# Kernel tuning notes

Measured on AMD Instinct MI355X. Metric: run time of the kernel, lower is better.

Reference implementation:

```python
import jax, jax.numpy as jnp
import numpy as np

NEG_SLOPE = 0.01  # torch F.leaky_relu default


def _gat_stack(x, W, a1w, a1b, a2w, a2b):
    """One GAT stack over all heads.
    x: (B, N, F_in); W: (H, F_in, d); a1w/a2w: (H, d); a1b/a2b: (H,)
    returns (B, N, H*d) -- heads concatenated in order along last dim.
    """
    # 1x1 conv1d (no bias) == per-node linear projection
    fts = jnp.einsum('bnf,hfd->hbnd', x, W)                      # (H,B,N,d)
    f1 = jnp.einsum('hbnd,hd->hbn', fts, a1w) + a1b[:, None, None]
    f2 = jnp.einsum('hbnd,hd->hbn', fts, a2w) + a2b[:, None, None]
    # logits[h,b,i,j] = f1[h,b,i] + f2[h,b,j]  (f_1.permute + f_2 broadcast)
    logits = f1[:, :, :, None] + f2[:, :, None, :]               # (H,B,N,N)
    coefs = jax.nn.softmax(jax.nn.leaky_relu(logits, NEG_SLOPE), axis=-1)
    vals = jnp.einsum('hbnm,hbmd->hbnd', coefs, fts)             # bmm aggregation
    ret = jax.nn.elu(vals + fts)                                 # residual-within-head + ELU activation
    B, N = x.shape[0], x.shape[1]
    return jnp.transpose(ret, (1, 2, 0, 3)).reshape(B, N, -1)    # cat(heads, dim=-1)


def setup_inputs() -> dict:
    key = jax.random.key(0)
    ks = jax.random.split(key, 7)
    B, N, F_in, H, d = 32, 512, 128, 8, 64
    hidden = H * d  # 512
    s = 0.05
    return {
        'x':   jax.random.normal(ks[0], (B, N, F_in), jnp.float32),
        'W0':  jax.random.normal(ks[1], (H, F_in, d), jnp.float32) * s,
        'W1':  jax.random.normal(ks[2], (H, hidden, d), jnp.float32) * s,
        'a1w': jax.random.normal(ks[3], (2, H, d), jnp.float32) * s,
        'a1b': jax.random.normal(ks[4], (2, H), jnp.float32) * s,
        'a2w': jax.random.normal(ks[5], (2, H, d), jnp.float32) * s,
        'a2b': jax.random.normal(ks[6], (2, H), jnp.float32) * s,
    }


def reference(x, W0, W1, a1w, a1b, a2w, a2b):
    # stack 0: input dim = num_random_sample
    h = _gat_stack(x, W0, a1w[0], a1b[0], a2w[0], a2b[0])
    # stack 1: input dim = hidden_dim
    out = _gat_stack(h, W1, a1w[1], a1b[1], a2w[1], a2b[1])
    return out
```

## Files before the change

### kernel.cpp

```cpp
#include <hip/hip_runtime.h>
#include <hip/hip_bf16.h>
#include <stdint.h>

typedef __attribute__((ext_vector_type(8))) short short8;
typedef __attribute__((ext_vector_type(4))) float f32x4;

#define L2E 1.44269504f
#define FN  131072

__device__ __forceinline__ short f2bf(float f) {
    unsigned u = __builtin_bit_cast(unsigned, f);
    return (short)((u + 0x8000u) >> 16);
}
__device__ __forceinline__ float bf2f(short s) {
    unsigned u = ((unsigned)(unsigned short)s) << 16;
    return __builtin_bit_cast(float, u);
}

__device__ __forceinline__ void gld16(void* l, const void* g) {
    __builtin_amdgcn_global_load_lds(
        (const __attribute__((address_space(1))) unsigned*)g,
        (__attribute__((address_space(3))) unsigned*)l, 16, 0, 0);
}

__global__ void wtrans_kernel(const float* __restrict__ W0, const float* __restrict__ W1,
                              short* __restrict__ BT0, short* __restrict__ BT1) {
    int idx = blockIdx.x * 256 + threadIdx.x;
    if (idx < 8 * 128 * 64) {
        int h = idx >> 13;
        int k = (idx >> 6) & 127;
        int dd = idx & 63;
        BT0[(h * 64 + dd) * 128 + k] = f2bf(W0[idx]);
    } else {
        int j = idx - 8 * 128 * 64;
        int h = j >> 15;
        int k = (j >> 6) & 511;
        int dd = j & 63;
        BT1[(h * 64 + dd) * 512 + k] = f2bf(W1[j]);
    }
}

template <typename AT>
__global__ __launch_bounds__(256, 2)
void gemm_kernel(const AT* __restrict__ A, const short* __restrict__ BT,
                 short* __restrict__ fts, int K,
                 const float* __restrict__ a1w, const float* __restrict__ a1b,
                 const float* __restrict__ a2w, const float* __restrict__ a2b,
                 float* __restrict__ fbuf) {
    __shared__ __align__(16) short As[128 * 64];
    __shared__ __align__(16) short Bs[128 * 64];

    const int tid  = threadIdx.x;
    const int lane = tid & 63;
    const int w    = tid >> 6;
    const int wr   = w >> 1, wc = w & 1;
    const int quad = lane >> 4, l15 = lane & 15;
    const int m0   = blockIdx.y * 128;
    const int n0   = blockIdx.x * 128;

    const int rl   = lane >> 3;
    const int cpos = lane & 7;
    const int kcl  = cpos ^ rl;

    f32x4 acc[4][4];
    for (int i = 0; i < 4; ++i)
        for (int j = 0; j < 4; ++j) { f32x4 z = {0.f, 0.f, 0.f, 0.f}; acc[i][j] = z; }

    const int nkb = K >> 6;
    for (int kb = 0; kb < nkb; ++kb) {
        __syncthreads();
        if constexpr (sizeof(AT) == 4) {
            for (int i = 0; i < 8; ++i) {
                int id  = tid + i * 256;
                int row = id >> 4, q = id & 15;
                int c = q >> 1, half = q & 1;
                float4 v = *(const float4*)((const float*)A + (size_t)(m0 + row) * K + kb * 64 + q * 4);
                ushort4 p;
                p.x = (unsigned short)f2bf(v.x);
                p.y = (unsigned short)f2bf(v.y);
                p.z = (unsigned short)f2bf(v.z);
                p.w = (unsigned short)f2bf(v.w);
                int swz = c ^ (row & 7);
                *(ushort4*)(As + row * 64 + swz * 8 + half * 4) = p;
            }
        } else {
            for (int i = 0; i < 4; ++i) {
                int rowb = w * 32 + i * 8;
                gld16(As + rowb * 64,
                      (const short*)A + (size_t)(m0 + rowb + rl) * K + kb * 64 + kcl * 8);
            }
        }
        for (int i = 0; i < 4; ++i) {
            int rowb = w * 32 + i * 8;
            gld16(Bs + rowb * 64,
                  BT + (size_t)(n0 + rowb + rl) * K + kb * 64 + kcl * 8);
        }
        __syncthreads();
        short8 af[2][4], bf[2][4];
        for (int ks = 0; ks < 2; ++ks) {
            for (int mf = 0; mf < 4; ++mf) {
                int row = wr * 64 + mf * 16 + l15;
                af[ks][mf] = *(const short8*)(As + row * 64 + (((ks * 4 + quad) ^ (row & 7)) << 3));
            }
            for (int nf = 0; nf < 4; ++nf) {
                int row = wc * 64 + nf * 16 + l15;
                bf[ks][nf] = *(const short8*)(Bs + row * 64 + (((ks * 4 + quad) ^ (row & 7)) << 3));
            }
        }
        for (int ks = 0; ks < 2; ++ks)
            for (int mf = 0; mf < 4; ++mf)
                for (int nf = 0; nf < 4; ++nf)
                    acc[mf][nf] = __builtin_amdgcn_mfma_f32_16x16x32_bf16(af[ks][mf], bf[ks][nf], acc[mf][nf], 0, 0, 0);
    }

    for (int nf = 0; nf < 4; ++nf) {
        int col = n0 + wc * 64 + nf * 16 + l15;
        int h = col >> 6, dd = col & 63;
        for (int mf = 0; mf < 4; ++mf) {
            int m = m0 + wr * 64 + mf * 16 + quad * 4;
            int b = m >> 9, n = m & 511;
            ushort4 pk;
            pk.x = (unsigned short)f2bf(acc[mf][nf][0]);
            pk.y = (unsigned short)f2bf(acc[mf][nf][1]);
            pk.z = (unsigned short)f2bf(acc[mf][nf][2]);
            pk.w = (unsigned short)f2bf(acc[mf][nf][3]);
            *(ushort4*)(fts + (size_t)((h * 32 + b) * 64 + dd) * 512 + n) = pk;
        }
    }

    {
        const int head = (n0 >> 6) + wc;
        float w1[4], w2[4];
        for (int nf = 0; nf < 4; ++nf) {
            w1[nf] = a1w[head * 64 + nf * 16 + l15];
            w2[nf] = a2w[head * 64 + nf * 16 + l15];
        }
        const float b1 = a1b[head], b2 = a2b[head];
        const int rsel = l15 & 3;
        for (int mf = 0; mf < 4; ++mf) {
            float g1[4], g2[4];
            for (int r = 0; r < 4; ++r) {
                float s1 = 0.f, s2 = 0.f;
                for (int nf = 0; nf < 4; ++nf) {
                    s1 += acc[mf][nf][r] * w1[nf];
                    s2 += acc[mf][nf][r] * w2[nf];
                }
                for (int m = 1; m < 16; m <<= 1) {
                    s1 += __shfl_xor(s1, m, 64);
                    s2 += __shfl_xor(s2, m, 64);
                }
                g1[r] = s1; g2[r] = s2;
            }
            float v1 = rsel == 0 ? g1[0] : rsel == 1 ? g1[1] : rsel == 2 ? g1[2] : g1[3];
            float v2 = rsel == 0 ? g2[0] : rsel == 1 ? g2[1] : rsel == 2 ? g2[2] : g2[3];
            if (l15 < 4) {
                int m = m0 + wr * 64 + mf * 16 + quad * 4 + rsel;
                int b = m >> 9, i = m & 511;
                int fi = (head * 32 + b) * 512 + i;
                float f1 = v1 + b1, f2 = v2 + b2;
                fbuf[0 * FN + fi] = __builtin_amdgcn_exp2f(f1 * L2E);
                fbuf[1 * FN + fi] = __builtin_amdgcn_exp2f(f1 * (0.01f * L2E));
                fbuf[2 * FN + fi] = __builtin_amdgcn_exp2f(f2 * L2E);
                fbuf[3 * FN + fi] = __builtin_amdgcn_exp2f(f2 * (0.01f * L2E));
            }
        }
    }
}

template <typename OutT>
__global__ __launch_bounds__(256, 4)
void attn_kernel(const short* __restrict__ fts, const float* __restrict__ fbuf,
                 OutT* __restrict__ out) {
    __shared__ __align__(16) short fb0[64 * 128];
    __shared__ __align__(16) short fb1[64 * 128];
    __shared__ __align__(16) float p2_s[512];
    __shared__ __align__(16) float q2_s[512];

    const int tid  = threadIdx.x;
    const int lane = tid & 63, w = tid >> 6;
    const int quad = lane >> 4, l15 = lane & 15;
    const int bx   = blockIdx.x;
    const int quarter = bx >> 8;
    const int slab = bx & 255;
    const int h    = slab >> 5;
    const int b    = slab & 31;
    const int r0   = quarter * 128;
    const size_t fbase = (size_t)(slab * 64) * 512;
    const int fidx = slab * 512;

    const int srow = lane >> 4;
    const int spc  = lane & 15;

    f32x4 acc[2][4], accL[2];
    for (int i = 0; i < 2; ++i) {
        f32x4 z = {0.f, 0.f, 0.f, 0.f};
        accL[i] = z;
        for (int j = 0; j < 4; ++j) acc[i][j] = z;
    }
    short8 onesv;
    for (int t = 0; t < 8; ++t) onesv[t] = (short)0x3F80;

    float P1r[2], Q1r[2];
    for (int rt = 0; rt < 2; ++rt) {
        int i = fidx + r0 + w * 32 + rt * 16 + l15;
        P1r[rt] = fbuf[i];
        Q1r[rt] = fbuf[1 * FN + i];
    }

    const float* p2g = fbuf + 2 * FN + fidx;
    const float* q2g = fbuf + 3 * FN + fidx;

    if (w < 2) gld16(p2_s + w * 256, p2g + w * 256 + lane * 4);
    else       gld16(q2_s + (w - 2) * 256, q2g + (w - 2) * 256 + lane * 4);

    auto stage = [&](int tc, short* buf) {
#pragma unroll
        for (int i = 0; i < 4; ++i) {
            int d0 = w * 16 + i * 4;
            int d  = d0 + srow;
            gld16(buf + d0 * 128,
                  fts + fbase + (size_t)d * 512 + tc * 128 + ((spc ^ (d & 7)) << 3));
        }
    };
    stage(0, fb0);
    stage(1, fb1);

#pragma unroll
    for (int tc = 0; tc < 4; ++tc) {
        if (tc < 3) asm volatile("s_waitcnt vmcnt(4)" ::: "memory");
        else        asm volatile("s_waitcnt vmcnt(0)" ::: "memory");
        __builtin_amdgcn_s_barrier();

        const short* buf = (tc & 1) ? fb1 : fb0;
#pragma unroll
        for (int jb = 0; jb < 4; ++jb) {
            short8 bfr[4];
#pragma unroll
            for (int nf = 0; nf < 4; ++nf) {
                int col = nf * 16 + l15;
                bfr[nf] = *(const short8*)(buf + col * 128 + (((jb * 4 + quad) ^ (col & 7)) << 3));
            }
            int o = tc * 128 + jb * 32 + quad * 8;
            f32x4 pa = *(const f32x4*)(p2_s + o), pb = *(const f32x4*)(p2_s + o + 4);
            f32x4 qa = *(const f32x4*)(q2_s + o), qb = *(const f32x4*)(q2_s + o + 4);
            float p2v[8] = {pa[0], pa[1], pa[2], pa[3], pb[0], pb[1], pb[2], pb[3]};
            float q2v[8] = {qa[0], qa[1], qa[2], qa[3], qb[0], qb[1], qb[2], qb[3]};

#pragma unroll
            for (int rt = 0; rt < 2; ++rt) {
                short8 ef;
#pragma unroll
                for (int t = 0; t < 8; ++t)
                    ef[t] = f2bf(fmaxf(P1r[rt] * p2v[t], Q1r[rt] * q2v[t]));
                for (int nf = 0; nf < 4; ++nf)
                    acc[rt][nf] = __builtin_amdgcn_mfma_f32_16x16x32_bf16(ef, bfr[nf], acc[rt][nf], 0, 0, 0);
                accL[rt] = __builtin_amdgcn_mfma_f32_16x16x32_bf16(ef, onesv, accL[rt], 0, 0, 0);
            }
        }

        __builtin_amdgcn_s_barrier();
        if (tc == 0) stage(2, fb0);
        if (tc == 1) stage(3, fb1);
    }

    for (int rt = 0; rt < 2; ++rt) {
        float rinv[4];
        for (int r = 0; r < 4; ++r) rinv[r] = __builtin_amdgcn_rcpf(accL[rt][r]);
        int i0 = r0 + w * 32 + rt * 16 + quad * 4;
        for (int nf = 0; nf < 4; ++nf) {
            int col = nf * 16 + l15;
            ushort4 res = *(const ushort4*)(fts + fbase + col * 512 + i0);
            unsigned short rr[4] = {res.x, res.y, res.z, res.w};
            for (int r = 0; r < 4; ++r) {
                float val = acc[rt][nf][r] * rinv[r] + bf2f((short)rr[r]);
                if (val < 0.f) val = __builtin_amdgcn_exp2f(val * L2E) - 1.f;
                size_t oidx = (size_t)(b * 512 + i0 + r) * 512 + h * 64 + col;
                if constexpr (sizeof(OutT) == 4) out[oidx] = val;
                else                             out[oidx] = f2bf(val);
            }
        }
    }
}

extern "C" void kernel_launch(void* const* d_in, const int* in_sizes, int n_in,
                              void* d_out, int out_size, void* d_ws, size_t ws_size,
                              hipStream_t stream) {
    const float* x   = (const float*)d_in[0];
    const float* W0  = (const float*)d_in[1];
    const float* W1  = (const float*)d_in[2];
    const float* a1w = (const float*)d_in[3];
    const float* a1b = (const float*)d_in[4];
    const float* a2w = (const float*)d_in[5];
    const float* a2b = (const float*)d_in[6];
    float* out = (float*)d_out;

    char* ws = (char*)d_ws;
    short* BT0  = (short*)(ws);
    short* BT1  = (short*)(ws + 131072);
    float* fbuf = (float*)(ws + 655360);
    short* fts  = (short*)(ws + 2752512);
    short* hbuf = (short*)d_out;

    wtrans_kernel<<<1280, 256, 0, stream>>>(W0, W1, BT0, BT1);

    gemm_kernel<float><<<dim3(4, 128), 256, 0, stream>>>(x, BT0, fts, 128,
                                                         a1w, a1b, a2w, a2b, fbuf);
    attn_kernel<short><<<1024, 256, 0, stream>>>(fts, fbuf, hbuf);

    gemm_kernel<short><<<dim3(4, 128), 256, 0, stream>>>(hbuf, BT1, fts, 512,
                                                         a1w + 512, a1b + 8, a2w + 512, a2b + 8, fbuf);
    attn_kernel<float><<<1024, 256, 0, stream>>>(fts, fbuf, out);
}
```

Measured before the change: 154.2 us.

## Double-buffer bf16 GEMM K-loop, swizzle block order, fence attention pipeline stages

For the bf16-input GEMM (second stack), A and B tiles are now double-buffered in LDS. The next K tile's async global-to-LDS loads are issued while MFMAs run on the current tile, so load latency is hidden instead of sitting behind a full barrier. The grid is flattened and remapped so that neighbouring blocks share A rows, which should improve L2 reuse. The attention kernel's barriers are wrapped in sched_barrier and lgkmcnt fences so the compiler cannot reorder LDS reads across the stage boundaries. In exchange, LDS use doubles to 64KB per block, which may limit occupancy.

```diff
diff --git a/kernel.cpp b/kernel.cpp
--- a/kernel.cpp
+++ b/kernel.cpp
@@ -22,6 +22,13 @@
         (const __attribute__((address_space(1))) unsigned*)g,
         (__attribute__((address_space(3))) unsigned*)l, 16, 0, 0);
 }
+
+#define PIPE_OPEN()  do { __builtin_amdgcn_s_barrier();                        \
+                          __builtin_amdgcn_sched_barrier(0);                   \
+                          asm volatile("" ::: "memory"); } while (0)
+#define PIPE_CLOSE() do { asm volatile("s_waitcnt lgkmcnt(0)" ::: "memory");   \
+                          __builtin_amdgcn_sched_barrier(0);                   \
+                          __builtin_amdgcn_s_barrier(); } while (0)
 
 __global__ void wtrans_kernel(const float* __restrict__ W0, const float* __restrict__ W1,
                               short* __restrict__ BT0, short* __restrict__ BT1) {
@@ -47,16 +54,20 @@
                  const float* __restrict__ a1w, const float* __restrict__ a1b,
                  const float* __restrict__ a2w, const float* __restrict__ a2b,
                  float* __restrict__ fbuf) {
-    __shared__ __align__(16) short As[128 * 64];
-    __shared__ __align__(16) short Bs[128 * 64];
+    __shared__ __align__(16) short As[2][128 * 64];
+    __shared__ __align__(16) short Bs[2][128 * 64];
 
     const int tid  = threadIdx.x;
     const int lane = tid & 63;
     const int w    = tid >> 6;
     const int wr   = w >> 1, wc = w & 1;
     const int quad = lane >> 4, l15 = lane & 15;
-    const int m0   = blockIdx.y * 128;
-    const int n0   = blockIdx.x * 128;
+
+    const int id = blockIdx.x;
+    const int bx = (id >> 3) & 3;
+    const int by = ((id >> 5) << 3) + (id & 7);
+    const int m0 = by * 128;
+    const int n0 = bx * 128;
 
     const int rl   = lane >> 3;
     const int cpos = lane & 7;
@@ -67,12 +78,13 @@
         for (int j = 0; j < 4; ++j) { f32x4 z = {0.f, 0.f, 0.f, 0.f}; acc[i][j] = z; }
 
     const int nkb = K >> 6;
-    for (int kb = 0; kb < nkb; ++kb) {
-        __syncthreads();
-        if constexpr (sizeof(AT) == 4) {
+
+    if constexpr (sizeof(AT) == 4) {
+        for (int kb = 0; kb < nkb; ++kb) {
+            __syncthreads();
             for (int i = 0; i < 8; ++i) {
-                int id  = tid + i * 256;
-                int row = id >> 4, q = id & 15;
+                int id2 = tid + i * 256;
+                int row = id2 >> 4, q = id2 & 15;
                 int c = q >> 1, half = q & 1;
                 float4 v = *(const float4*)((const float*)A + (size_t)(m0 + row) * K + kb * 64 + q * 4);
                 ushort4 p;
@@ -81,36 +93,71 @@
                 p.z = (unsigned short)f2bf(v.z);
                 p.w = (unsigned short)f2bf(v.w);
                 int swz = c ^ (row & 7);
-                *(ushort4*)(As + row * 64 + swz * 8 + half * 4) = p;
-            }
-        } else {
+                *(ushort4*)(As[0] + row * 64 + swz * 8 + half * 4) = p;
+            }
             for (int i = 0; i < 4; ++i) {
                 int rowb = w * 32 + i * 8;
-                gld16(As + rowb * 64,
+                gld16(Bs[0] + rowb * 64,
+                      BT + (size_t)(n0 + rowb + rl) * K + kb * 64 + kcl * 8);
+            }
+            __syncthreads();
+            short8 af[2][4], bf[2][4];
+            for (int ks = 0; ks < 2; ++ks) {
+                for (int mf = 0; mf < 4; ++mf) {
+                    int row = wr * 64 + mf * 16 + l15;
+                    af[ks][mf] = *(const short8*)(As[0] + row * 64 + (((ks * 4 + quad) ^ (row & 7)) << 3));
+                }
+                for (int nf = 0; nf < 4; ++nf) {
+                    int row = wc * 64 + nf * 16 + l15;
+                    bf[ks][nf] = *(const short8*)(Bs[0] + row * 64 + (((ks * 4 + quad) ^ (row & 7)) << 3));
+                }
+            }
+            for (int ks = 0; ks < 2; ++ks)
+                for (int mf = 0; mf < 4; ++mf)
+                    for (int nf = 0; nf < 4; ++nf)
+                        acc[mf][nf] = __builtin_amdgcn_mfma_f32_16x16x32_bf16(af[ks][mf], bf[ks][nf], acc[mf][nf], 0, 0, 0);
+        }
+    } else {
+        auto stageAB = [&](int kb, int bufi) {
+#pragma unroll
+            for (int i = 0; i < 4; ++i) {
+                int rowb = w * 32 + i * 8;
+                gld16(As[bufi] + rowb * 64,
                       (const short*)A + (size_t)(m0 + rowb + rl) * K + kb * 64 + kcl * 8);
             }
-        }
-        for (int i = 0; i < 4; ++i) {
-            int rowb = w * 32 + i * 8;
-            gld16(Bs + rowb * 64,
-                  BT + (size_t)(n0 + rowb + rl) * K + kb * 64 + kcl * 8);
-        }
-        __syncthreads();
-        short8 af[2][4], bf[2][4];
-        for (int ks = 0; ks < 2; ++ks) {
-            for (int mf = 0; mf < 4; ++mf) {
-                int row = wr * 64 + mf * 16 + l15;
-                af[ks][mf] = *(const short8*)(As + row * 64 + (((ks * 4 + quad) ^ (row & 7)) << 3));
-            }
-            for (int nf = 0; nf < 4; ++nf) {
-                int row = wc * 64 + nf * 16 + l15;
-                bf[ks][nf] = *(const short8*)(Bs + row * 64 + (((ks * 4 + quad) ^ (row & 7)) << 3));
-            }
-        }
-        for (int ks = 0; ks < 2; ++ks)
-            for (int mf = 0; mf < 4; ++mf)
-                for (int nf = 0; nf < 4; ++nf)
-                    acc[mf][nf] = __builtin_amdgcn_mfma_f32_16x16x32_bf16(af[ks][mf], bf[ks][nf], acc[mf][nf], 0, 0, 0);
+#pragma unroll
+            for (int i = 0; i < 4; ++i) {
+                int rowb = w * 32 + i * 8;
+                gld16(Bs[bufi] + rowb * 64,
+                      BT + (size_t)(n0 + rowb + rl) * K + kb * 64 + kcl * 8);
+            }
+        };
+        stageAB(0, 0);
+        if (nkb > 1) stageAB(1, 1);
+        for (int kb = 0; kb < nkb; ++kb) {
+            if (kb + 1 < nkb) asm volatile("s_waitcnt vmcnt(8)" ::: "memory");
+            else              asm volatile("s_waitcnt vmcnt(0)" ::: "memory");
+            PIPE_OPEN();
+            const short* as = As[kb & 1];
+            const short* bs = Bs[kb & 1];
+            short8 af[2][4], bf[2][4];
+            for (int ks = 0; ks < 2; ++ks) {
+                for (int mf = 0; mf < 4; ++mf) {
+                    int row = wr * 64 + mf * 16 + l15;
+                    af[ks][mf] = *(const short8*)(as + row * 64 + (((ks * 4 + quad) ^ (row & 7)) << 3));
+                }
+                for (int nf = 0; nf < 4; ++nf) {
+                    int row = wc * 64 + nf * 16 + l15;
+                    bf[ks][nf] = *(const short8*)(bs + row * 64 + (((ks * 4 + quad) ^ (row & 7)) << 3));
+                }
+            }
+            for (int ks = 0; ks < 2; ++ks)
+                for (int mf = 0; mf < 4; ++mf)
+                    for (int nf = 0; nf < 4; ++nf)
+                        acc[mf][nf] = __builtin_amdgcn_mfma_f32_16x16x32_bf16(af[ks][mf], bf[ks][nf], acc[mf][nf], 0, 0, 0);
+            PIPE_CLOSE();
+            if (kb + 2 < nkb) stageAB(kb + 2, kb & 1);
+        }
     }
 
     for (int nf = 0; nf < 4; ++nf) {
@@ -229,7 +276,7 @@
     for (int tc = 0; tc < 4; ++tc) {
         if (tc < 3) asm volatile("s_waitcnt vmcnt(4)" ::: "memory");
         else        asm volatile("s_waitcnt vmcnt(0)" ::: "memory");
-        __builtin_amdgcn_s_barrier();
+        PIPE_OPEN();
 
         const short* buf = (tc & 1) ? fb1 : fb0;
 #pragma unroll
@@ -258,7 +305,7 @@
             }
         }
 
-        __builtin_amdgcn_s_barrier();
+        PIPE_CLOSE();
         if (tc == 0) stage(2, fb0);
         if (tc == 1) stage(3, fb1);
     }
@@ -303,11 +350,11 @@
 
     wtrans_kernel<<<1280, 256, 0, stream>>>(W0, W1, BT0, BT1);
 
-    gemm_kernel<float><<<dim3(4, 128), 256, 0, stream>>>(x, BT0, fts, 128,
-                                                         a1w, a1b, a2w, a2b, fbuf);
+    gemm_kernel<float><<<512, 256, 0, stream>>>(x, BT0, fts, 128,
+                                                a1w, a1b, a2w, a2b, fbuf);
     attn_kernel<short><<<1024, 256, 0, stream>>>(fts, fbuf, hbuf);
 
-    gemm_kernel<short><<<dim3(4, 128), 256, 0, stream>>>(hbuf, BT1, fts, 512,
-                                                         a1w + 512, a1b + 8, a2w + 512, a2b + 8, fbuf);
+    gemm_kernel<short><<<512, 256, 0, stream>>>(hbuf, BT1, fts, 512,
+                                                a1w + 512, a1b + 8, a2w + 512, a2b + 8, fbuf);
     attn_kernel<float><<<1024, 256, 0, stream>>>(fts, fbuf, out);
 }
```

After: 145.4 us. -5.7%, faster.
